# Performance work log

Hardware: AMD Instinct MI355X
Metric: run time of the kernel (lower is better)

The kernel has to match this reference:

```python
import jax, jax.numpy as jnp
import numpy as np

EPS = 1e-8  # EPS is referenced but undefined in the original source; standard small epsilon


def setup_inputs() -> dict:
    key = jax.random.key(0)
    ks = jax.random.split(key, 12)
    B, T, F = 8, 512, 512
    H, maxlen = 8, 1024
    dh = F // H
    s = 0.02
    return {
        "x": jax.random.normal(ks[0], (B, T, F), jnp.float32),
        "Wq": jax.random.normal(ks[1], (F, F), jnp.float32) * s,
        "bq": jax.random.normal(ks[2], (F,), jnp.float32) * s,
        "Wk": jax.random.normal(ks[3], (F, F), jnp.float32) * s,
        "bk": jax.random.normal(ks[4], (F,), jnp.float32) * s,
        "Wv": jax.random.normal(ks[5], (F, F), jnp.float32) * s,
        "bv": jax.random.normal(ks[6], (F,), jnp.float32) * s,
        "Wo": jax.random.normal(ks[7], (F, F), jnp.float32) * s,
        "bo": jax.random.normal(ks[8], (F,), jnp.float32) * s,
        "delta": jnp.ones((1,), jnp.float32),
        "cache_k": jax.random.normal(ks[9], (B * H, maxlen, dh), jnp.float32),
        "cache_v": jax.random.normal(ks[10], (B * H, maxlen, dh), jnp.float32),
    }


def _to_heads(y, B, T, H, dh):
    # torch.cat(torch.split(y, dh, dim=-1), dim=0): head-major (H*B, T, dh)
    return y.reshape(B, T, H, dh).transpose(2, 0, 1, 3).reshape(H * B, T, dh)


def reference(x, Wq, bq, Wk, bk, Wv, bv, Wo, bo, delta, cache_k, cache_v):
    B, T, F = x.shape
    maxlen, dh = cache_k.shape[1], cache_k.shape[2]
    H = F // dh

    q = _to_heads(x @ Wq.T + bq, B, T, H, dh)  # (HB, T, dh)
    k_new = _to_heads(x @ Wk.T + bk, B, T, H, dh)
    v_new = _to_heads(x @ Wv.T + bv, B, T, H, dh)

    # streaming cache: drop oldest T frames, append new
    k = jnp.concatenate([cache_k[:, T:], k_new], axis=1)  # (HB, maxlen, dh)
    v = jnp.concatenate([cache_v[:, T:], v_new], axis=1)

    # Gaussian relative-position mask G[i,j] = exp(-(i-j)^2 / (delta^2 + EPS))
    ind = jnp.arange(1, maxlen + 1, dtype=x.dtype)
    diff = ind[:, None] - ind[None, :]
    G = jnp.exp(-(diff ** 2) / (delta[0] ** 2 + EPS))  # (maxlen, maxlen)

    d = jnp.sqrt(jnp.asarray(F, jnp.float32)).astype(x.dtype)
    scores = jnp.einsum("btd,bsd->bts", q, k) * G[-T:][None] / d  # (HB, T, maxlen)
    attn = jax.nn.softmax(scores, axis=-1)
    out = jnp.einsum("bts,bsd->btd", attn, v)  # (HB, T, dh)

    # undo head-major split: cat(split(out, B, dim=0), dim=-1)
    out = out.reshape(H, B, T, dh).transpose(1, 2, 0, 3).reshape(B, T, F)
    return out @ Wo.T + bo
```

## Files before the change

kernel.cpp:

```cpp
#include <hip/hip_runtime.h>

typedef __bf16 bf16;
typedef __bf16 bf16x8 __attribute__((ext_vector_type(8)));
typedef __bf16 bf16x4 __attribute__((ext_vector_type(4)));
typedef float f32x4 __attribute__((ext_vector_type(4)));
typedef float f32x16 __attribute__((ext_vector_type(16)));

#define MFMA16(a, b, c) __builtin_amdgcn_mfma_f32_16x16x32_bf16((a), (b), (c), 0, 0, 0)
#define MFMA32(a, b, c) __builtin_amdgcn_mfma_f32_32x32x16_bf16((a), (b), (c), 0, 0, 0)

__device__ __forceinline__ void gload_lds16(const void* g, void* l) {
  __builtin_amdgcn_global_load_lds(
      (const __attribute__((address_space(1))) void*)g,
      (__attribute__((address_space(3))) void*)l, 16, 0, 0);
}

__global__ __launch_bounds__(256) void cvt_f32_bf16(const float* __restrict__ s,
                                                    bf16* __restrict__ d, int n) {
  int i = (blockIdx.x * 256 + threadIdx.x) * 4;
  const int stride = gridDim.x * 256 * 4;
  for (; i < n; i += stride) {
    f32x4 v = *(const f32x4*)(s + i);
    bf16x4 o;
    o[0] = (bf16)v[0]; o[1] = (bf16)v[1]; o[2] = (bf16)v[2]; o[3] = (bf16)v[3];
    *(bf16x4*)(d + i) = o;
  }
}

__global__ __launch_bounds__(256) void cvt_w4(const float* __restrict__ w0, const float* __restrict__ w1,
                                              const float* __restrict__ w2, const float* __restrict__ w3,
                                              bf16* __restrict__ o0, bf16* __restrict__ o1,
                                              bf16* __restrict__ o2, bf16* __restrict__ o3,
                                              const float* __restrict__ delta, float* __restrict__ gt) {
  const int y = blockIdx.y;
  if (y == 4) {
    int i = blockIdx.x * 256 + threadIdx.x;
    if (i < 1535) {
      float dl = delta[0];
      float inv = 1.0f / (dl * dl + 1e-8f);
      float diff = (float)(i - 511);
      gt[i] = __expf(-diff * diff * inv) * 0.04419417382415922f;
    }
    return;
  }
  const float* s = y == 0 ? w0 : y == 1 ? w1 : y == 2 ? w2 : w3;
  bf16* d = y == 0 ? o0 : y == 1 ? o1 : y == 2 ? o2 : o3;
  int i = (blockIdx.x * 256 + threadIdx.x) * 4;
  f32x4 v = *(const f32x4*)(s + i);
  bf16x4 o;
  o[0] = (bf16)v[0]; o[1] = (bf16)v[1]; o[2] = (bf16)v[2]; o[3] = (bf16)v[3];
  *(bf16x4*)(d + i) = o;
}

__global__ __launch_bounds__(256) void cache_prep(const float* __restrict__ ck,
                                                  const float* __restrict__ cv,
                                                  bf16* __restrict__ kk,
                                                  bf16* __restrict__ vt) {
  const int hb = blockIdx.y;
  const int st = blockIdx.x;
  const int tid = threadIdx.x;
  __shared__ bf16 tl[64][65];
  const int s0 = st * 64;
#pragma unroll
  for (int it = 0; it < 16; ++it) {
    int idx = it * 256 + tid;
    int sl = idx >> 6, dd = idx & 63;
    float kval = ck[((size_t)hb * 1024 + 512 + s0 + sl) * 64 + dd];
    kk[((size_t)hb * 1024 + s0 + sl) * 64 + dd] = (bf16)kval;
    float vval = cv[((size_t)hb * 1024 + 512 + s0 + sl) * 64 + dd];
    tl[sl][dd] = (bf16)vval;
  }
  __syncthreads();
#pragma unroll
  for (int it = 0; it < 16; ++it) {
    int idx = it * 256 + tid;
    int dl = idx >> 6, sl = idx & 63;
    vt[((size_t)hb * 64 + dl) * 1024 + s0 + sl] = tl[sl][dl];
  }
}

__global__ __launch_bounds__(256) void qkv_gemm(const bf16* __restrict__ xb,
                                                const bf16* __restrict__ wq, const bf16* __restrict__ wk,
                                                const bf16* __restrict__ wv,
                                                const float* __restrict__ bq, const float* __restrict__ bk,
                                                const float* __restrict__ bv,
                                                bf16* __restrict__ qh, bf16* __restrict__ kk,
                                                bf16* __restrict__ vt) {
  __shared__ bf16 As[64 * 32];
  __shared__ bf16 Bs[64 * 32];
  const int tid = threadIdx.x;
  const int lane = tid & 63;
  const int wave = tid >> 6;
  const int wr = wave >> 1, wc = wave & 1;
  const int l15 = lane & 15, lg = lane >> 4;
  const int mbase = blockIdx.x * 64;
  const int nfull = blockIdx.y * 64;
  const int mid = nfull >> 9;
  const int nbase = nfull & 511;
  const bf16* W = mid == 0 ? wq : (mid == 1 ? wk : wv);
  const float* bias = mid == 0 ? bq : (mid == 1 ? bk : bv);
  f32x4 acc[2][2] = {};

  const int o = tid * 16;
  const int row = o >> 6;
  const int cb = o & 63;
  for (int k0 = 0; k0 < 512; k0 += 32) {
    __syncthreads();
    gload_lds16((const char*)(xb + (size_t)(mbase + row) * 512 + k0) + cb, (char*)As + o);
    gload_lds16((const char*)(W + (size_t)(nbase + row) * 512 + k0) + cb, (char*)Bs + o);
    __syncthreads();
    bf16x8 af[2], bfr[2];
#pragma unroll
    for (int i = 0; i < 2; ++i)
      af[i] = *(const bf16x8*)(As + (wr * 32 + i * 16 + l15) * 32 + lg * 8);
#pragma unroll
    for (int j = 0; j < 2; ++j)
      bfr[j] = *(const bf16x8*)(Bs + (wc * 32 + j * 16 + l15) * 32 + lg * 8);
#pragma unroll
    for (int i = 0; i < 2; ++i)
#pragma unroll
      for (int j = 0; j < 2; ++j)
        acc[i][j] = MFMA16(af[i], bfr[j], acc[i][j]);
  }

#pragma unroll
  for (int j = 0; j < 2; ++j) {
    const int nn = nbase + wc * 32 + j * 16 + l15;
    const float bvv = bias[nn];
    const int h = nn >> 6, dd = nn & 63;
#pragma unroll
    for (int i = 0; i < 2; ++i) {
#pragma unroll
      for (int r = 0; r < 4; ++r) {
        const int mr = mbase + wr * 32 + i * 16 + lg * 4 + r;
        const float v = acc[i][j][r] + bvv;
        const int bb = mr >> 9, t = mr & 511;
        if (mid == 0) {
          qh[(((size_t)(h * 8 + bb) * 512 + t) << 6) + dd] = (bf16)v;
        } else if (mid == 1) {
          kk[(((size_t)(h * 8 + bb) * 1024 + 512 + t) << 6) + dd] = (bf16)v;
        } else {
          vt[(((size_t)(h * 8 + bb) * 64 + dd) << 10) + 512 + t] = (bf16)v;
        }
      }
    }
  }
}

__global__ __launch_bounds__(256) void out_gemm(const bf16* __restrict__ A,
                                                const bf16* __restrict__ W,
                                                const float* __restrict__ bias,
                                                float* __restrict__ out) {
  __shared__ bf16 As[64 * 32];
  __shared__ bf16 Bs[64 * 32];
  const int tid = threadIdx.x;
  const int lane = tid & 63;
  const int wave = tid >> 6;
  const int wr = wave >> 1, wc = wave & 1;
  const int l15 = lane & 15, lg = lane >> 4;
  const int mbase = blockIdx.x * 64;
  const int nbase = blockIdx.y * 64;
  f32x4 acc[2][2] = {};

  const int o = tid * 16;
  const int row = o >> 6;
  const int cb = o & 63;
  for (int k0 = 0; k0 < 512; k0 += 32) {
    __syncthreads();
    gload_lds16((const char*)(A + (size_t)(mbase + row) * 512 + k0) + cb, (char*)As + o);
    gload_lds16((const char*)(W + (size_t)(nbase + row) * 512 + k0) + cb, (char*)Bs + o);
    __syncthreads();
    bf16x8 af[2], bfr[2];
#pragma unroll
    for (int i = 0; i < 2; ++i)
      af[i] = *(const bf16x8*)(As + (wr * 32 + i * 16 + l15) * 32 + lg * 8);
#pragma unroll
    for (int j = 0; j < 2; ++j)
      bfr[j] = *(const bf16x8*)(Bs + (wc * 32 + j * 16 + l15) * 32 + lg * 8);
#pragma unroll
    for (int i = 0; i < 2; ++i)
#pragma unroll
      for (int j = 0; j < 2; ++j)
        acc[i][j] = MFMA16(af[i], bfr[j], acc[i][j]);
  }

#pragma unroll
  for (int j = 0; j < 2; ++j) {
    const int nn = nbase + wc * 32 + j * 16 + l15;
    const float bvv = bias[nn];
#pragma unroll
    for (int i = 0; i < 2; ++i) {
#pragma unroll
      for (int r = 0; r < 4; ++r) {
        const int mr = mbase + wr * 32 + i * 16 + lg * 4 + r;
        out[(size_t)mr * 512 + nn] = acc[i][j][r] + bvv;
      }
    }
  }
}

__global__ __launch_bounds__(256) void attn_k(const bf16* __restrict__ qh,
                                              const bf16* __restrict__ kk,
                                              const bf16* __restrict__ vt,
                                              const float* __restrict__ gtab,
                                              bf16* __restrict__ ao) {
  const int bid = blockIdx.x;
  const int xcd = bid & 7;
  const int g = bid >> 3;
  const int hb = xcd * 8 + (g >> 3);
  const int qp = g & 7;
  const int tid = threadIdx.x;
  const int lane = tid & 63;
  const int wave = tid >> 6;
  const int l31 = lane & 31;
  const int hi = lane >> 5;
  const int qtile = qp * 2 + (wave & 1);
  const int kvhalf = wave >> 1;
  const int qbase = qtile * 32;
  const int t = qbase + l31;

  __shared__ float gl[1536];
  __shared__ __align__(16) bf16 pbuf[4][32][40];
  __shared__ float mbuf[2][64][33];
  __shared__ float mlb[2][64][2];

  for (int i = tid; i < 1535; i += 256) gl[i] = gtab[i];

  const bf16* qrow = qh + ((size_t)hb * 512 + t) * 64 + hi * 8;
  bf16x8 qf0 = *(const bf16x8*)(qrow);
  bf16x8 qf1 = *(const bf16x8*)(qrow + 16);
  bf16x8 qf2 = *(const bf16x8*)(qrow + 32);
  bf16x8 qf3 = *(const bf16x8*)(qrow + 48);

  const bf16* kbase = kk + (size_t)hb * 1024 * 64;
  const bf16* vbase = vt + (size_t)hb * 64 * 1024;
  const bf16* krow = kbase + (size_t)l31 * 64 + hi * 8;
  const bf16* vrow = vbase + (size_t)l31 * 1024 + hi * 8;

  const int sb0 = kvhalf * 512;
  float m_r = -3.0e38f, l_r = 0.f;
  f32x16 accA = {}, accB = {};

  __syncthreads();

  bf16x8 kc0, kc1, kc2, kc3, kn0, kn1, kn2, kn3;
  {
    const bf16* kp = krow + (size_t)sb0 * 64;
    kc0 = *(const bf16x8*)(kp);
    kc1 = *(const bf16x8*)(kp + 16);
    kc2 = *(const bf16x8*)(kp + 32);
    kc3 = *(const bf16x8*)(kp + 48);
  }

#define ATTN_STEP(C0, C1, C2, C3, N0, N1, N2, N3, SB, PF)                       \
  {                                                                             \
    f32x16 c = {};                                                              \
    c = MFMA32(C0, qf0, c);                                                     \
    c = MFMA32(C1, qf1, c);                                                     \
    c = MFMA32(C2, qf2, c);                                                     \
    c = MFMA32(C3, qf3, c);                                                     \
    if (PF) {                                         \
      const bf16* kp_ = krow + (size_t)((SB) + 32) * 64;                        \
      N0 = *(const bf16x8*)(kp_);                                               \
      N1 = *(const bf16x8*)(kp_ + 16);                                          \
      N2 = *(const bf16x8*)(kp_ + 32);                                          \
      N3 = *(const bf16x8*)(kp_ + 48);                                          \
    }                                                                           \
                                                   \
    const bf16* vp_ = vrow + (SB);                                              \
    bf16x8 vf00 = *(const bf16x8*)(vp_);                                        \
    bf16x8 vf01 = *(const bf16x8*)(vp_ + 16);                                   \
    bf16x8 vf10 = *(const bf16x8*)(vp_ + 32768);                                \
    bf16x8 vf11 = *(const bf16x8*)(vp_ + 32768 + 16);                           \
                \
    const int BASE = 1023 + t - (SB)-4 * hi;                                    \
    float x[16];                                                                \
    _Pragma("unroll") for (int gq = 0; gq < 4; ++gq)                            \
        _Pragma("unroll") for (int j = 0; j < 4; ++j)                           \
            x[gq * 4 + j] = c[gq * 4 + j] * gl[BASE - 8 * gq - j];              \
    float pm = x[0];                                                            \
    _Pragma("unroll") for (int r = 1; r < 16; ++r) pm = fmaxf(pm, x[r]);        \
    pm = fmaxf(pm, __shfl_xor(pm, 32, 64));                                     \
    const float mn = fmaxf(m_r, pm);                                            \
    const float fac = __expf(m_r - mn);                                         \
    m_r = mn;                                                                   \
    float ps = 0.f;                                                             \
    float e[16];                                                                \
    _Pragma("unroll") for (int r = 0; r < 16; ++r) {                            \
      e[r] = __expf(x[r] - mn);                                                 \
      ps += e[r];                                                               \
    }                                                                           \
                      \
    _Pragma("unroll") for (int gq = 0; gq < 4; ++gq) {                          \
      bf16x4 pw;                                                                \
      _Pragma("unroll") for (int j = 0; j < 4; ++j) pw[j] = (bf16)e[gq * 4 + j];\
      *(bf16x4*)&pbuf[wave][l31][4 * hi + 8 * gq] = pw;                         \
    }                                                                           \
    ps += __shfl_xor(ps, 32, 64);                                               \
    l_r = l_r * fac + ps;                                                       \
    _Pragma("unroll") for (int r = 0; r < 16; ++r) {                            \
      accA[r] *= fac;                                                           \
      accB[r] *= fac;                                                           \
    }                                                                           \
    asm volatile("s_waitcnt lgkmcnt(0)" ::: "memory");                          \
    __builtin_amdgcn_sched_barrier(0);                                          \
                  \
    bf16x8 P0 = *(const bf16x8*)&pbuf[wave][l31][8 * hi];                       \
    bf16x8 P1 = *(const bf16x8*)&pbuf[wave][l31][16 + 8 * hi];                  \
    accA = MFMA32(vf00, P0, accA);                                              \
    accA = MFMA32(vf01, P1, accA);                                              \
    accB = MFMA32(vf10, P0, accB);                                              \
    accB = MFMA32(vf11, P1, accB);                                              \
  }

  int sb = sb0;
#pragma unroll 1
  for (int it2 = 0; it2 < 8; ++it2) {
    ATTN_STEP(kc0, kc1, kc2, kc3, kn0, kn1, kn2, kn3, sb, true);
    ATTN_STEP(kn0, kn1, kn2, kn3, kc0, kc1, kc2, kc3, sb + 32, it2 < 7);
    sb += 64;
  }
#undef ATTN_STEP

  __syncthreads();
  const int slot = wave & 1;
  if (kvhalf == 1) {
#pragma unroll
    for (int r = 0; r < 16; ++r) {
      mbuf[slot][lane][r] = accA[r];
      mbuf[slot][lane][16 + r] = accB[r];
    }
    mlb[slot][lane][0] = m_r;
    mlb[slot][lane][1] = l_r;
  }
  __syncthreads();
  if (kvhalf == 0) {
    const float mp = mlb[slot][lane][0];
    const float lp = mlb[slot][lane][1];
    const float M = fmaxf(m_r, mp);
    const float f0 = __expf(m_r - M);
    const float f1 = __expf(mp - M);
    const float linv = 1.0f / (l_r * f0 + lp * f1);
    const int b = hb & 7, h = hb >> 3;
    bf16* obase = ao + ((size_t)(b * 512 + t) * 512) + h * 64;
#pragma unroll
    for (int D = 0; D < 2; ++D) {
#pragma unroll
      for (int gq = 0; gq < 4; ++gq) {
        bf16x4 ov;
#pragma unroll
        for (int j = 0; j < 4; ++j) {
          const float own = D ? accB[gq * 4 + j] : accA[gq * 4 + j];
          const float oth = mbuf[slot][lane][D * 16 + gq * 4 + j];
          ov[j] = (bf16)((own * f0 + oth * f1) * linv);
        }
        *(bf16x4*)(obase + D * 32 + gq * 8 + hi * 4) = ov;
      }
    }
  }
}

extern "C" void kernel_launch(void* const* d_in, const int* in_sizes, int n_in,
                              void* d_out, int out_size, void* d_ws, size_t ws_size,
                              hipStream_t stream) {
  const float* x = (const float*)d_in[0];
  const float* Wq = (const float*)d_in[1];
  const float* bq = (const float*)d_in[2];
  const float* Wk = (const float*)d_in[3];
  const float* bk = (const float*)d_in[4];
  const float* Wv = (const float*)d_in[5];
  const float* bv = (const float*)d_in[6];
  const float* Wo = (const float*)d_in[7];
  const float* bo = (const float*)d_in[8];
  const float* delta = (const float*)d_in[9];
  const float* ck = (const float*)d_in[10];
  const float* cv = (const float*)d_in[11];

  char* w = (char*)d_ws;
  auto carve = [&](size_t bytes) {
    char* p = w;
    w += (bytes + 255) & ~(size_t)255;
    return p;
  };
  bf16* xb = (bf16*)carve((size_t)4096 * 512 * 2);
  bf16* wqb = (bf16*)carve((size_t)512 * 512 * 2);
  bf16* wkb = (bf16*)carve((size_t)512 * 512 * 2);
  bf16* wvb = (bf16*)carve((size_t)512 * 512 * 2);
  bf16* wob = (bf16*)carve((size_t)512 * 512 * 2);
  bf16* qhb = (bf16*)carve((size_t)64 * 512 * 64 * 2);
  bf16* kkb = (bf16*)carve((size_t)64 * 1024 * 64 * 2);
  bf16* vtb = (bf16*)carve((size_t)64 * 64 * 1024 * 2);
  bf16* aob = (bf16*)carve((size_t)4096 * 512 * 2);
  float* gt = (float*)carve(1536 * 4);

  cvt_f32_bf16<<<2048, 256, 0, stream>>>(x, xb, 4096 * 512);
  cvt_w4<<<dim3(256, 5), 256, 0, stream>>>(Wq, Wk, Wv, Wo, wqb, wkb, wvb, wob, delta, gt);
  cache_prep<<<dim3(8, 64), 256, 0, stream>>>(ck, cv, kkb, vtb);
  qkv_gemm<<<dim3(64, 24), 256, 0, stream>>>(xb, wqb, wkb, wvb, bq, bk, bv, qhb, kkb, vtb);
  attn_k<<<512, 256, 0, stream>>>(qhb, kkb, vtb, gt, aob);
  out_gemm<<<dim3(64, 8), 256, 0, stream>>>(aob, wob, bo, (float*)d_out);
}
```

Before: 78.21 us.

## Merge prep kernels, widen QKV GEMM tile, and add lazy exp2 softmax rescaling

Three separate preprocessing launches (x conversion, weight conversion with the Gaussian table, cache copy and transpose) become one kernel dispatched by block index. This removes two launches and their gaps. The QKV GEMM tile grows to 128 rows per block, so each wave computes a 32x64 slab and B-tile reuse improves, at the price of half as many blocks. The attention softmax now folds log2(e) into the Gaussian table and uses exp2f, and it skips the running-max rescale of the accumulators unless some lane's max rises by more than 12, which saves multiplies but lets unscaled values grow up to 2^12.

```diff
diff --git a/kernel.cpp b/kernel.cpp
--- a/kernel.cpp
+++ b/kernel.cpp
@@ -15,67 +15,61 @@
       (__attribute__((address_space(3))) void*)l, 16, 0, 0);
 }
 
-__global__ __launch_bounds__(256) void cvt_f32_bf16(const float* __restrict__ s,
-                                                    bf16* __restrict__ d, int n) {
-  int i = (blockIdx.x * 256 + threadIdx.x) * 4;
-  const int stride = gridDim.x * 256 * 4;
-  for (; i < n; i += stride) {
+__global__ __launch_bounds__(256) void prep_all(
+    const float* __restrict__ x, const float* __restrict__ w0, const float* __restrict__ w1,
+    const float* __restrict__ w2, const float* __restrict__ w3, const float* __restrict__ delta,
+    const float* __restrict__ ck, const float* __restrict__ cv,
+    bf16* __restrict__ xb, bf16* __restrict__ o0, bf16* __restrict__ o1,
+    bf16* __restrict__ o2, bf16* __restrict__ o3, float* __restrict__ gt,
+    bf16* __restrict__ kk, bf16* __restrict__ vt) {
+  const int bid = blockIdx.x;
+  const int tid = threadIdx.x;
+  __shared__ bf16 tl[64][65];
+
+  if (bid < 2048) {
+    const int i = (bid * 256 + tid) * 4;
+    f32x4 v = *(const f32x4*)(x + i);
+    bf16x4 o;
+    o[0] = (bf16)v[0]; o[1] = (bf16)v[1]; o[2] = (bf16)v[2]; o[3] = (bf16)v[3];
+    *(bf16x4*)(xb + i) = o;
+  } else if (bid < 3072) {
+    const int wb = bid - 2048;
+    const int widx = wb >> 8;
+    const float* s = widx == 0 ? w0 : widx == 1 ? w1 : widx == 2 ? w2 : w3;
+    bf16* d = widx == 0 ? o0 : widx == 1 ? o1 : widx == 2 ? o2 : o3;
+    const int i = ((wb & 255) * 256 + tid) * 4;
     f32x4 v = *(const f32x4*)(s + i);
     bf16x4 o;
     o[0] = (bf16)v[0]; o[1] = (bf16)v[1]; o[2] = (bf16)v[2]; o[3] = (bf16)v[3];
     *(bf16x4*)(d + i) = o;
-  }
-}
-
-__global__ __launch_bounds__(256) void cvt_w4(const float* __restrict__ w0, const float* __restrict__ w1,
-                                              const float* __restrict__ w2, const float* __restrict__ w3,
-                                              bf16* __restrict__ o0, bf16* __restrict__ o1,
-                                              bf16* __restrict__ o2, bf16* __restrict__ o3,
-                                              const float* __restrict__ delta, float* __restrict__ gt) {
-  const int y = blockIdx.y;
-  if (y == 4) {
-    int i = blockIdx.x * 256 + threadIdx.x;
+  } else if (bid < 3584) {
+    const int b2 = bid - 3072;
+    const int hb = b2 >> 3;
+    const int s0 = (b2 & 7) * 64;
+#pragma unroll
+    for (int it = 0; it < 16; ++it) {
+      int idx = it * 256 + tid;
+      int sl = idx >> 6, dd = idx & 63;
+      float kval = ck[((size_t)hb * 1024 + 512 + s0 + sl) * 64 + dd];
+      kk[((size_t)hb * 1024 + s0 + sl) * 64 + dd] = (bf16)kval;
+      float vval = cv[((size_t)hb * 1024 + 512 + s0 + sl) * 64 + dd];
+      tl[sl][dd] = (bf16)vval;
+    }
+    __syncthreads();
+#pragma unroll
+    for (int it = 0; it < 16; ++it) {
+      int idx = it * 256 + tid;
+      int dl = idx >> 6, sl = idx & 63;
+      vt[((size_t)hb * 64 + dl) * 1024 + s0 + sl] = tl[sl][dl];
+    }
+  } else {
+    const int i = (bid - 3584) * 256 + tid;
     if (i < 1535) {
       float dl = delta[0];
       float inv = 1.0f / (dl * dl + 1e-8f);
       float diff = (float)(i - 511);
-      gt[i] = __expf(-diff * diff * inv) * 0.04419417382415922f;
-    }
-    return;
-  }
-  const float* s = y == 0 ? w0 : y == 1 ? w1 : y == 2 ? w2 : w3;
-  bf16* d = y == 0 ? o0 : y == 1 ? o1 : y == 2 ? o2 : o3;
-  int i = (blockIdx.x * 256 + threadIdx.x) * 4;
-  f32x4 v = *(const f32x4*)(s + i);
-  bf16x4 o;
-  o[0] = (bf16)v[0]; o[1] = (bf16)v[1]; o[2] = (bf16)v[2]; o[3] = (bf16)v[3];
-  *(bf16x4*)(d + i) = o;
-}
-
-__global__ __launch_bounds__(256) void cache_prep(const float* __restrict__ ck,
-                                                  const float* __restrict__ cv,
-                                                  bf16* __restrict__ kk,
-                                                  bf16* __restrict__ vt) {
-  const int hb = blockIdx.y;
-  const int st = blockIdx.x;
-  const int tid = threadIdx.x;
-  __shared__ bf16 tl[64][65];
-  const int s0 = st * 64;
-#pragma unroll
-  for (int it = 0; it < 16; ++it) {
-    int idx = it * 256 + tid;
-    int sl = idx >> 6, dd = idx & 63;
-    float kval = ck[((size_t)hb * 1024 + 512 + s0 + sl) * 64 + dd];
-    kk[((size_t)hb * 1024 + s0 + sl) * 64 + dd] = (bf16)kval;
-    float vval = cv[((size_t)hb * 1024 + 512 + s0 + sl) * 64 + dd];
-    tl[sl][dd] = (bf16)vval;
-  }
-  __syncthreads();
-#pragma unroll
-  for (int it = 0; it < 16; ++it) {
-    int idx = it * 256 + tid;
-    int dl = idx >> 6, sl = idx & 63;
-    vt[((size_t)hb * 64 + dl) * 1024 + s0 + sl] = tl[sl][dl];
+      gt[i] = __expf(-diff * diff * inv) * 0.04419417382415922f * 1.4426950408889634f;
+    }
   }
 }
 
@@ -86,53 +80,57 @@
                                                 const float* __restrict__ bv,
                                                 bf16* __restrict__ qh, bf16* __restrict__ kk,
                                                 bf16* __restrict__ vt) {
-  __shared__ bf16 As[64 * 32];
+  __shared__ bf16 As[128 * 32];
   __shared__ bf16 Bs[64 * 32];
   const int tid = threadIdx.x;
   const int lane = tid & 63;
   const int wave = tid >> 6;
-  const int wr = wave >> 1, wc = wave & 1;
   const int l15 = lane & 15, lg = lane >> 4;
-  const int mbase = blockIdx.x * 64;
+  const int mbase = blockIdx.x * 128;
   const int nfull = blockIdx.y * 64;
   const int mid = nfull >> 9;
   const int nbase = nfull & 511;
   const bf16* W = mid == 0 ? wq : (mid == 1 ? wk : wv);
   const float* bias = mid == 0 ? bq : (mid == 1 ? bk : bv);
-  f32x4 acc[2][2] = {};
-
-  const int o = tid * 16;
-  const int row = o >> 6;
-  const int cb = o & 63;
+  f32x4 acc[2][4] = {};
+
+  const int oB = tid * 16;
+  const int rowB = oB >> 6;
+  const int cbB = oB & 63;
   for (int k0 = 0; k0 < 512; k0 += 32) {
     __syncthreads();
-    gload_lds16((const char*)(xb + (size_t)(mbase + row) * 512 + k0) + cb, (char*)As + o);
-    gload_lds16((const char*)(W + (size_t)(nbase + row) * 512 + k0) + cb, (char*)Bs + o);
+#pragma unroll
+    for (int t = 0; t < 2; ++t) {
+      const int oA = (t * 256 + tid) * 16;
+      gload_lds16((const char*)(xb + (size_t)(mbase + (oA >> 6)) * 512 + k0) + (oA & 63),
+                  (char*)As + oA);
+    }
+    gload_lds16((const char*)(W + (size_t)(nbase + rowB) * 512 + k0) + cbB, (char*)Bs + oB);
     __syncthreads();
-    bf16x8 af[2], bfr[2];
+    bf16x8 af[2], bfr[4];
 #pragma unroll
     for (int i = 0; i < 2; ++i)
-      af[i] = *(const bf16x8*)(As + (wr * 32 + i * 16 + l15) * 32 + lg * 8);
-#pragma unroll
-    for (int j = 0; j < 2; ++j)
-      bfr[j] = *(const bf16x8*)(Bs + (wc * 32 + j * 16 + l15) * 32 + lg * 8);
+      af[i] = *(const bf16x8*)(As + (wave * 32 + i * 16 + l15) * 32 + lg * 8);
+#pragma unroll
+    for (int j = 0; j < 4; ++j)
+      bfr[j] = *(const bf16x8*)(Bs + (j * 16 + l15) * 32 + lg * 8);
 #pragma unroll
     for (int i = 0; i < 2; ++i)
 #pragma unroll
-      for (int j = 0; j < 2; ++j)
+      for (int j = 0; j < 4; ++j)
         acc[i][j] = MFMA16(af[i], bfr[j], acc[i][j]);
   }
 
 #pragma unroll
-  for (int j = 0; j < 2; ++j) {
-    const int nn = nbase + wc * 32 + j * 16 + l15;
+  for (int j = 0; j < 4; ++j) {
+    const int nn = nbase + j * 16 + l15;
     const float bvv = bias[nn];
     const int h = nn >> 6, dd = nn & 63;
 #pragma unroll
     for (int i = 0; i < 2; ++i) {
 #pragma unroll
       for (int r = 0; r < 4; ++r) {
-        const int mr = mbase + wr * 32 + i * 16 + lg * 4 + r;
+        const int mr = mbase + wave * 32 + i * 16 + lg * 4 + r;
         const float v = acc[i][j][r] + bvv;
         const int bb = mr >> 9, t = mr & 511;
         if (mid == 0) {
@@ -272,7 +270,7 @@
     bf16x8 vf01 = *(const bf16x8*)(vp_ + 16);                                   \
     bf16x8 vf10 = *(const bf16x8*)(vp_ + 32768);                                \
     bf16x8 vf11 = *(const bf16x8*)(vp_ + 32768 + 16);                           \
-                \
+     \
     const int BASE = 1023 + t - (SB)-4 * hi;                                    \
     float x[16];                                                                \
     _Pragma("unroll") for (int gq = 0; gq < 4; ++gq)                            \
@@ -281,13 +279,20 @@
     float pm = x[0];                                                            \
     _Pragma("unroll") for (int r = 1; r < 16; ++r) pm = fmaxf(pm, x[r]);        \
     pm = fmaxf(pm, __shfl_xor(pm, 32, 64));                                     \
-    const float mn = fmaxf(m_r, pm);                                            \
-    const float fac = __expf(m_r - mn);                                         \
-    m_r = mn;                                                                   \
+    if (!__all(pm <= m_r + 12.0f)) {             \
+      const float mn = fmaxf(m_r, pm);                                          \
+      const float fac = exp2f(m_r - mn);                                        \
+      m_r = mn;                                                                 \
+      l_r *= fac;                                                               \
+      _Pragma("unroll") for (int r = 0; r < 16; ++r) {                          \
+        accA[r] *= fac;                                                         \
+        accB[r] *= fac;                                                         \
+      }                                                                         \
+    }                                                                           \
     float ps = 0.f;                                                             \
     float e[16];                                                                \
     _Pragma("unroll") for (int r = 0; r < 16; ++r) {                            \
-      e[r] = __expf(x[r] - mn);                                                 \
+      e[r] = exp2f(x[r] - m_r);                                                 \
       ps += e[r];                                                               \
     }                                                                           \
                       \
@@ -297,11 +302,7 @@
       *(bf16x4*)&pbuf[wave][l31][4 * hi + 8 * gq] = pw;                         \
     }                                                                           \
     ps += __shfl_xor(ps, 32, 64);                                               \
-    l_r = l_r * fac + ps;                                                       \
-    _Pragma("unroll") for (int r = 0; r < 16; ++r) {                            \
-      accA[r] *= fac;                                                           \
-      accB[r] *= fac;                                                           \
-    }                                                                           \
+    l_r += ps;                                                                  \
     asm volatile("s_waitcnt lgkmcnt(0)" ::: "memory");                          \
     __builtin_amdgcn_sched_barrier(0);                                          \
                   \
@@ -338,8 +339,8 @@
     const float mp = mlb[slot][lane][0];
     const float lp = mlb[slot][lane][1];
     const float M = fmaxf(m_r, mp);
-    const float f0 = __expf(m_r - M);
-    const float f1 = __expf(mp - M);
+    const float f0 = exp2f(m_r - M);
+    const float f1 = exp2f(mp - M);
     const float linv = 1.0f / (l_r * f0 + lp * f1);
     const int b = hb & 7, h = hb >> 3;
     bf16* obase = ao + ((size_t)(b * 512 + t) * 512) + h * 64;
@@ -393,10 +394,9 @@
   bf16* aob = (bf16*)carve((size_t)4096 * 512 * 2);
   float* gt = (float*)carve(1536 * 4);
 
-  cvt_f32_bf16<<<2048, 256, 0, stream>>>(x, xb, 4096 * 512);
-  cvt_w4<<<dim3(256, 5), 256, 0, stream>>>(Wq, Wk, Wv, Wo, wqb, wkb, wvb, wob, delta, gt);
-  cache_prep<<<dim3(8, 64), 256, 0, stream>>>(ck, cv, kkb, vtb);
-  qkv_gemm<<<dim3(64, 24), 256, 0, stream>>>(xb, wqb, wkb, wvb, bq, bk, bv, qhb, kkb, vtb);
+  prep_all<<<3590, 256, 0, stream>>>(x, Wq, Wk, Wv, Wo, delta, ck, cv,
+                                     xb, wqb, wkb, wvb, wob, gt, kkb, vtb);
+  qkv_gemm<<<dim3(32, 24), 256, 0, stream>>>(xb, wqb, wkb, wvb, bq, bk, bv, qhb, kkb, vtb);
   attn_k<<<512, 256, 0, stream>>>(qhb, kkb, vtb, gt, aob);
   out_gemm<<<dim3(64, 8), 256, 0, stream>>>(aob, wob, bo, (float*)d_out);
 }
```

Result: faster. 71.64 us (median of 4 runs) (-8.4%).
